# Kernel optimization log

Hardware: AMD Instinct MI355X
Metric: run time of the kernel (lower is better)

Reference implementation:

```python
import jax, jax.numpy as jnp
import numpy as np

E = 8        # num_experts
TOP_K = 2    # num_experts_per_tok
H = 2048     # hidden_size
I = 1408     # moe_intermediate_size

def setup_inputs() -> dict:
    key = jax.random.key(0)
    k0, k1, k2, k3, k4 = jax.random.split(key, 5)
    hidden_states = jax.random.normal(k0, (2, 2048, H), dtype=jnp.float32)
    gate_w = jax.random.normal(k1, (E, H), dtype=jnp.float32) * 0.02   # router: Linear(H, E)
    wg = jax.random.normal(k2, (E, I, H), dtype=jnp.float32) * 0.02    # gate_proj per expert
    wu = jax.random.normal(k3, (E, I, H), dtype=jnp.float32) * 0.02    # up_proj per expert
    wd = jax.random.normal(k4, (E, H, I), dtype=jnp.float32) * 0.02    # down_proj per expert
    return {"hidden_states": hidden_states, "gate_w": gate_w, "wg": wg, "wu": wu, "wd": wd}

def reference(hidden_states, gate_w, wg, wu, wd):
    b, s, h = hidden_states.shape
    x = hidden_states.reshape(-1, h)                      # [T, H]
    router_logits = x @ gate_w.T                          # [T, E]
    routing_weights = jax.nn.softmax(router_logits.astype(jnp.float32), axis=-1)
    topk_weight, topk_idx = jax.lax.top_k(routing_weights, TOP_K)   # [T, K]
    topk_weight = topk_weight / jnp.sum(topk_weight, axis=-1, keepdims=True)
    # per-token combine weight for each expert: w[t,e] = sum_k topk_weight[t,k] * [topk_idx[t,k]==e]
    comb = jnp.sum(jax.nn.one_hot(topk_idx, E, dtype=x.dtype) * topk_weight[..., None].astype(x.dtype), axis=1)  # [T, E]
    # compute each expert on all tokens (dense faithful equivalent of masked dispatch), combine with comb
    def expert_out(e):
        g = x @ wg[e].T                                   # [T, I]
        u = x @ wu[e].T                                   # [T, I]
        return (jax.nn.silu(g) * u) @ wd[e].T             # [T, H]
    y = jnp.zeros_like(x)
    for e in range(E):  # small fixed expert count
        y = y + expert_out(e) * comb[:, e:e+1]
    final = y.reshape(b, s, h)
    return final, router_logits.astype(hidden_states.dtype)
```

## Files before the change

kernel.cpp:

```cpp
#include <hip/hip_runtime.h>

#define NTOK 4096
#define NEXP 8
#define HD 2048
#define ID 1408

typedef unsigned short u16;
typedef __attribute__((ext_vector_type(8))) short short8;
typedef __attribute__((ext_vector_type(4))) short short4v;
typedef __attribute__((ext_vector_type(4))) float f32x4;
typedef const __attribute__((address_space(1))) void* gas_ptr;
typedef __attribute__((address_space(3))) void* las_ptr;

__device__ __forceinline__ u16 f2bf(float f) {
  unsigned int u = __float_as_uint(f);
  u += 0x7FFFu + ((u >> 16) & 1u);
  return (u16)(u >> 16);
}

__device__ __forceinline__ void async16(const u16* g, u16* l) {
  __builtin_amdgcn_global_load_lds((gas_ptr)g, (las_ptr)l, 16, 0, 0);
}

__global__ void cvt3_kernel(const float* __restrict__ s0, const float* __restrict__ s1,
                            const float* __restrict__ s2, u16* __restrict__ d0,
                            u16* __restrict__ d1, u16* __restrict__ d2, long n8each) {
  long i = (long)blockIdx.x * blockDim.x + threadIdx.x;
  const float* s; u16* d; long j;
  if (i < n8each)            { s = s0; d = d0; j = i; }
  else if (i < 2*n8each)     { s = s1; d = d1; j = i - n8each; }
  else if (i < 3*n8each)     { s = s2; d = d2; j = i - 2*n8each; }
  else return;
  const float4* s4 = (const float4*)s;
  float4 a = s4[2*j], b = s4[2*j+1];
  short8 o;
  o[0] = (short)f2bf(a.x); o[1] = (short)f2bf(a.y);
  o[2] = (short)f2bf(a.z); o[3] = (short)f2bf(a.w);
  o[4] = (short)f2bf(b.x); o[5] = (short)f2bf(b.y);
  o[6] = (short)f2bf(b.z); o[7] = (short)f2bf(b.w);
  *(short8*)(d + 8*j) = o;
}

__global__ void router_kernel(const float* __restrict__ x, const float* __restrict__ gw,
                              u16* __restrict__ xb,
                              float* __restrict__ logits, int* __restrict__ cnt,
                              int* __restrict__ ptok, float* __restrict__ pw) {
  int t = blockIdx.x * 4 + (threadIdx.x >> 6);
  int lane = threadIdx.x & 63;
  if (t >= NTOK) return;
  const float4* xr = (const float4*)(x + (size_t)t * HD);
  u16* xbr = xb + (size_t)t * HD;
  float dot[NEXP];
#pragma unroll
  for (int e = 0; e < NEXP; ++e) dot[e] = 0.f;
#pragma unroll
  for (int c = 0; c < 8; ++c) {
    float4 xv = xr[c*64 + lane];
    short4v o;
    o[0] = (short)f2bf(xv.x); o[1] = (short)f2bf(xv.y);
    o[2] = (short)f2bf(xv.z); o[3] = (short)f2bf(xv.w);
    *(short4v*)(xbr + (c*64 + lane)*4) = o;
#pragma unroll
    for (int e = 0; e < NEXP; ++e) {
      float4 gv = ((const float4*)(gw + e*HD))[c*64 + lane];
      dot[e] += xv.x*gv.x + xv.y*gv.y + xv.z*gv.z + xv.w*gv.w;
    }
  }
#pragma unroll
  for (int off = 32; off > 0; off >>= 1) {
#pragma unroll
    for (int e = 0; e < NEXP; ++e) dot[e] += __shfl_xor(dot[e], off);
  }
  if (lane < NEXP) logits[(size_t)t*NEXP + lane] = dot[lane];
  if (lane == 0) {
    float mx = dot[0];
#pragma unroll
    for (int e = 1; e < NEXP; ++e) mx = fmaxf(mx, dot[e]);
    float p[NEXP];
#pragma unroll
    for (int e = 0; e < NEXP; ++e) p[e] = __expf(dot[e] - mx);
    int e0 = 0;
#pragma unroll
    for (int e = 1; e < NEXP; ++e) if (p[e] > p[e0]) e0 = e;
    int e1 = (e0 == 0) ? 1 : 0;
#pragma unroll
    for (int e = 0; e < NEXP; ++e) if (e != e0 && p[e] > p[e1]) e1 = e;
    float denom = p[e0] + p[e1];
    int pos0 = atomicAdd(&cnt[e0], 1);
    ptok[e0*NTOK + pos0] = t; pw[e0*NTOK + pos0] = p[e0] / denom;
    int pos1 = atomicAdd(&cnt[e1], 1);
    ptok[e1*NTOK + pos1] = t; pw[e1*NTOK + pos1] = p[e1] / denom;
  }
}

__global__ void prefix_kernel(const int* __restrict__ cnt, int* __restrict__ offs) {
  if (threadIdx.x == 0) {
    int a = 0;
    for (int e = 0; e < NEXP; ++e) { offs[e] = a; a += cnt[e]; }
  }
}

__global__ __launch_bounds__(256, 2) void gemm1_kernel(
    const u16* __restrict__ xb, const u16* __restrict__ wgb, const u16* __restrict__ wub,
    const int* __restrict__ cnt, const int* __restrict__ offs,
    const int* __restrict__ ptok, u16* __restrict__ hbuf) {
  int e = blockIdx.z, mt = blockIdx.y, nt = blockIdx.x;
  int c = cnt[e];
  if (mt * 128 >= c) return;
  int off = offs[e];

  __shared__ u16 sA[128*64], sBg[128*64], sBu[128*64];

  int tid = threadIdx.x;
  int r  = tid >> 3;
  int cq = tid & 7;
  int cx = (cq ^ (r & 7)) * 8;

  const u16* ga[4];
#pragma unroll
  for (int p = 0; p < 4; ++p) {
    int s = mt*128 + r + p*32;
    int t = ptok[e*NTOK + (s < c ? s : 0)];
    ga[p] = xb + (size_t)t*HD + cx;
  }
  int n0 = nt*128 + r;
  const u16* gg = wgb + ((size_t)e*ID + n0)*HD + cx;
  const u16* gu = wub + ((size_t)e*ID + n0)*HD + cx;

  int lane = tid & 63, wv = tid >> 6, wr = wv >> 1, wc = wv & 1;
  int fm = lane & 15, kg = lane >> 4;
  int sw = fm & 7;

  f32x4 accg[4][4], accu[4][4];
#pragma unroll
  for (int i = 0; i < 4; ++i)
#pragma unroll
    for (int j = 0; j < 4; ++j) {
      accg[i][j] = {0.f, 0.f, 0.f, 0.f};
      accu[i][j] = {0.f, 0.f, 0.f, 0.f};
    }

  for (int k0 = 0; k0 < HD; k0 += 64) {
#pragma unroll
    for (int p = 0; p < 4; ++p) {
      async16(ga[p] + k0,                 sA  + p*2048 + tid*8);
      async16(gg + (size_t)p*32*HD + k0,  sBg + p*2048 + tid*8);
      async16(gu + (size_t)p*32*HD + k0,  sBu + p*2048 + tid*8);
    }
    __syncthreads();
#pragma unroll
    for (int h = 0; h < 2; ++h) {
      int co = ((kg + 4*h) ^ sw) * 8;
      short8 af[4], bg[4], bu[4];
#pragma unroll
      for (int i = 0; i < 4; ++i)
        af[i] = *(const short8*)(sA + (wr*64 + i*16 + fm)*64 + co);
#pragma unroll
      for (int j = 0; j < 4; ++j) {
        bg[j] = *(const short8*)(sBg + (wc*64 + j*16 + fm)*64 + co);
        bu[j] = *(const short8*)(sBu + (wc*64 + j*16 + fm)*64 + co);
      }
#pragma unroll
      for (int i = 0; i < 4; ++i)
#pragma unroll
        for (int j = 0; j < 4; ++j) {
          accg[i][j] = __builtin_amdgcn_mfma_f32_16x16x32_bf16(af[i], bg[j], accg[i][j], 0, 0, 0);
          accu[i][j] = __builtin_amdgcn_mfma_f32_16x16x32_bf16(af[i], bu[j], accu[i][j], 0, 0, 0);
        }
    }
    __syncthreads();
  }

#pragma unroll
  for (int i = 0; i < 4; ++i) {
#pragma unroll
    for (int rr = 0; rr < 4; ++rr) {
      int slot = mt*128 + wr*64 + i*16 + kg*4 + rr;
      if (slot < c) {
        size_t rowb = (size_t)(off + slot) * ID + nt*128 + wc*64 + fm;
#pragma unroll
        for (int j = 0; j < 4; ++j) {
          float gv = accg[i][j][rr], uv = accu[i][j][rr];
          float hh = gv * uv / (1.f + __expf(-gv));
          hbuf[rowb + (size_t)j*16] = f2bf(hh);
        }
      }
    }
  }
}

__global__ __launch_bounds__(256, 3) void gemm2_kernel(
    const u16* __restrict__ hbuf, const u16* __restrict__ wdb,
    const int* __restrict__ cnt, const int* __restrict__ offs,
    const int* __restrict__ ptok, const float* __restrict__ pw,
    float* __restrict__ out) {
  int e = blockIdx.z, mt = blockIdx.y, nt = blockIdx.x;
  int c = cnt[e];
  if (mt * 128 >= c) return;
  int off = offs[e];

  __shared__ u16 sA[128*64], sB[128*64];

  int tid = threadIdx.x;
  int r  = tid >> 3;
  int cq = tid & 7;
  int cx = (cq ^ (r & 7)) * 8;

  const u16* ga[4];
#pragma unroll
  for (int p = 0; p < 4; ++p) {
    int s = mt*128 + r + p*32;
    ga[p] = hbuf + (size_t)(off + (s < c ? s : 0))*ID + cx;
  }
  int n0 = nt*128 + r;
  const u16* gb = wdb + ((size_t)e*HD + n0)*ID + cx;

  int lane = tid & 63, wv = tid >> 6, wr = wv >> 1, wc = wv & 1;
  int fm = lane & 15, kg = lane >> 4;
  int sw = fm & 7;

  f32x4 acc[4][4];
#pragma unroll
  for (int i = 0; i < 4; ++i)
#pragma unroll
    for (int j = 0; j < 4; ++j) acc[i][j] = {0.f, 0.f, 0.f, 0.f};

  for (int k0 = 0; k0 < ID; k0 += 64) {
#pragma unroll
    for (int p = 0; p < 4; ++p) {
      async16(ga[p] + k0,                sA + p*2048 + tid*8);
      async16(gb + (size_t)p*32*ID + k0, sB + p*2048 + tid*8);
    }
    __syncthreads();
#pragma unroll
    for (int h = 0; h < 2; ++h) {
      int co = ((kg + 4*h) ^ sw) * 8;
      short8 af[4], bf[4];
#pragma unroll
      for (int i = 0; i < 4; ++i)
        af[i] = *(const short8*)(sA + (wr*64 + i*16 + fm)*64 + co);
#pragma unroll
      for (int j = 0; j < 4; ++j)
        bf[j] = *(const short8*)(sB + (wc*64 + j*16 + fm)*64 + co);
#pragma unroll
      for (int i = 0; i < 4; ++i)
#pragma unroll
        for (int j = 0; j < 4; ++j)
          acc[i][j] = __builtin_amdgcn_mfma_f32_16x16x32_bf16(af[i], bf[j], acc[i][j], 0, 0, 0);
    }
    __syncthreads();
  }

#pragma unroll
  for (int i = 0; i < 4; ++i) {
#pragma unroll
    for (int rr = 0; rr < 4; ++rr) {
      int slot = mt*128 + wr*64 + i*16 + kg*4 + rr;
      if (slot < c) {
        int tok = ptok[e*NTOK + slot];
        float wgt = pw[e*NTOK + slot];
        float* orow = out + (size_t)tok*HD + nt*128 + wc*64 + fm;
#pragma unroll
        for (int j = 0; j < 4; ++j)
          atomicAdd(orow + j*16, wgt * acc[i][j][rr]);
      }
    }
  }
}

extern "C" void kernel_launch(void* const* d_in, const int* in_sizes, int n_in,
                              void* d_out, int out_size, void* d_ws, size_t ws_size,
                              hipStream_t stream) {
  const float* x  = (const float*)d_in[0];
  const float* gw = (const float*)d_in[1];
  const float* wg = (const float*)d_in[2];
  const float* wu = (const float*)d_in[3];
  const float* wd = (const float*)d_in[4];
  float* out = (float*)d_out;

  char* p = (char*)d_ws;
  u16*   xb   = (u16*)(p);
  u16*   wgb  = (u16*)(p + 16777216UL);
  u16*   wub  = (u16*)(p + 62914560UL);
  u16*   wdb  = (u16*)(p + 109051904UL);
  u16*   hbuf = (u16*)(p + 155189248UL);
  int*   ptok = (int*)(p + 178257920UL);
  float* pww  = (float*)(p + 178388992UL);
  int*   cnt  = (int*)(p + 178520064UL);
  int*   offs = (int*)(p + 178520320UL);

  hipMemsetAsync(out, 0, (size_t)NTOK * HD * sizeof(float), stream);
  hipMemsetAsync(cnt, 0, NEXP * sizeof(int), stream);

  long n8each = (long)NEXP * ID * HD / 8;
  cvt3_kernel<<<33792, 256, 0, stream>>>(wg, wu, wd, wgb, wub, wdb, n8each);

  router_kernel<<<1024, 256, 0, stream>>>(x, gw, xb, out + (size_t)NTOK * HD, cnt, ptok, pww);
  prefix_kernel<<<1, 64, 0, stream>>>(cnt, offs);

  gemm1_kernel<<<dim3(11, 32, 8), 256, 0, stream>>>(xb, wgb, wub, cnt, offs, ptok, hbuf);
  gemm2_kernel<<<dim3(16, 32, 8), 256, 0, stream>>>(hbuf, wdb, cnt, offs, ptok, pww, out);
}
```

Before: 652.3 us.

## Double-buffer GEMM k-loops and split fused gate/up GEMM into two kernels

Introduces a shared double-buffered k-loop that prefetches the next two LDS tiles with async global-to-LDS loads, uses explicit waitcnt/barrier placement, and raises MFMA priority around the matrix-multiply blocks. The fused gate+up GEMM is split into a gate kernel, which writes bf16 gate values to hbuf, and an up kernel, which reads them back and applies SiLU*up. The split lowers register and LDS pressure per kernel but rereads x tiles, costs an extra hbuf round trip, and rounds the gate values to bf16 before the activation. The down-projection kernel also reuses the pipelined loop, with occupancy reduced from 3 to 2 blocks.

```diff
diff --git a/kernel.cpp b/kernel.cpp
--- a/kernel.cpp
+++ b/kernel.cpp
@@ -16,6 +16,9 @@
   unsigned int u = __float_as_uint(f);
   u += 0x7FFFu + ((u >> 16) & 1u);
   return (u16)(u >> 16);
+}
+__device__ __forceinline__ float bf2f(u16 v) {
+  return __uint_as_float((unsigned int)v << 16);
 }
 
 __device__ __forceinline__ void async16(const u16* g, u16* l) {
@@ -100,8 +103,74 @@
   }
 }
 
-__global__ __launch_bounds__(256, 2) void gemm1_kernel(
-    const u16* __restrict__ xb, const u16* __restrict__ wgb, const u16* __restrict__ wub,
+template<int NT>
+__device__ __forceinline__ void kloop(
+    const u16* const ga[4], const u16* const gb[4],
+    u16* sA, u16* sB, int tid, int fm, int kg, int wr, int wc,
+    f32x4 (&acc)[4][4])
+{
+  const int sw = fm & 7;
+  const int ar = wr*64 + fm;
+  const int br = wc*64 + fm;
+
+#define ISSUE(buf, k0) do { \
+    _Pragma("unroll") \
+    for (int p = 0; p < 4; ++p) { \
+      async16(ga[p] + (k0), sA + (buf)*8192 + p*2048 + tid*8); \
+      async16(gb[p] + (k0), sB + (buf)*8192 + p*2048 + tid*8); \
+    } } while (0)
+
+  ISSUE(0, 0);
+  ISSUE(1, 64);
+  asm volatile("s_waitcnt vmcnt(8)" ::: "memory");
+  asm volatile("s_barrier" ::: "memory");
+
+  for (int t = 0; t < NT; ++t) {
+    const u16* bA = sA + (t & 1) * 8192;
+    const u16* bB = sB + (t & 1) * 8192;
+    short8 a0[4], b0[4];
+    {
+      int co = (kg ^ sw) * 8;
+#pragma unroll
+      for (int i = 0; i < 4; ++i) a0[i] = *(const short8*)(bA + (ar + i*16)*64 + co);
+#pragma unroll
+      for (int j = 0; j < 4; ++j) b0[j] = *(const short8*)(bB + (br + j*16)*64 + co);
+    }
+    asm volatile("s_barrier" ::: "memory");
+    __builtin_amdgcn_s_setprio(1);
+#pragma unroll
+    for (int i = 0; i < 4; ++i)
+#pragma unroll
+      for (int j = 0; j < 4; ++j)
+        acc[i][j] = __builtin_amdgcn_mfma_f32_16x16x32_bf16(a0[i], b0[j], acc[i][j], 0, 0, 0);
+    __builtin_amdgcn_s_setprio(0);
+    asm volatile("s_barrier" ::: "memory");
+    short8 a1[4], b1[4];
+    {
+      int co = ((kg + 4) ^ sw) * 8;
+#pragma unroll
+      for (int i = 0; i < 4; ++i) a1[i] = *(const short8*)(bA + (ar + i*16)*64 + co);
+#pragma unroll
+      for (int j = 0; j < 4; ++j) b1[j] = *(const short8*)(bB + (br + j*16)*64 + co);
+    }
+    asm volatile("s_barrier" ::: "memory");
+    if (t + 2 < NT) ISSUE((t & 1), (t + 2) * 64);
+    __builtin_amdgcn_s_setprio(1);
+#pragma unroll
+    for (int i = 0; i < 4; ++i)
+#pragma unroll
+      for (int j = 0; j < 4; ++j)
+        acc[i][j] = __builtin_amdgcn_mfma_f32_16x16x32_bf16(a1[i], b1[j], acc[i][j], 0, 0, 0);
+    __builtin_amdgcn_s_setprio(0);
+    if (t < NT - 2)       asm volatile("s_waitcnt vmcnt(8)" ::: "memory");
+    else if (t == NT - 2) asm volatile("s_waitcnt vmcnt(0)" ::: "memory");
+    asm volatile("s_barrier" ::: "memory");
+  }
+#undef ISSUE
+}
+
+__global__ __launch_bounds__(256, 2) void gemmg_kernel(
+    const u16* __restrict__ xb, const u16* __restrict__ wgb,
     const int* __restrict__ cnt, const int* __restrict__ offs,
     const int* __restrict__ ptok, u16* __restrict__ hbuf) {
   int e = blockIdx.z, mt = blockIdx.y, nt = blockIdx.x;
@@ -109,7 +178,7 @@
   if (mt * 128 >= c) return;
   int off = offs[e];
 
-  __shared__ u16 sA[128*64], sBg[128*64], sBu[128*64];
+  __shared__ u16 sA[2*128*64], sB[2*128*64];
 
   int tid = threadIdx.x;
   int r  = tid >> 3;
@@ -123,53 +192,21 @@
     int t = ptok[e*NTOK + (s < c ? s : 0)];
     ga[p] = xb + (size_t)t*HD + cx;
   }
-  int n0 = nt*128 + r;
-  const u16* gg = wgb + ((size_t)e*ID + n0)*HD + cx;
-  const u16* gu = wub + ((size_t)e*ID + n0)*HD + cx;
+  const u16* gb[4];
+#pragma unroll
+  for (int p = 0; p < 4; ++p)
+    gb[p] = wgb + ((size_t)e*ID + nt*128 + r + p*32)*HD + cx;
 
   int lane = tid & 63, wv = tid >> 6, wr = wv >> 1, wc = wv & 1;
   int fm = lane & 15, kg = lane >> 4;
-  int sw = fm & 7;
-
-  f32x4 accg[4][4], accu[4][4];
+
+  f32x4 acc[4][4];
 #pragma unroll
   for (int i = 0; i < 4; ++i)
 #pragma unroll
-    for (int j = 0; j < 4; ++j) {
-      accg[i][j] = {0.f, 0.f, 0.f, 0.f};
-      accu[i][j] = {0.f, 0.f, 0.f, 0.f};
-    }
-
-  for (int k0 = 0; k0 < HD; k0 += 64) {
-#pragma unroll
-    for (int p = 0; p < 4; ++p) {
-      async16(ga[p] + k0,                 sA  + p*2048 + tid*8);
-      async16(gg + (size_t)p*32*HD + k0,  sBg + p*2048 + tid*8);
-      async16(gu + (size_t)p*32*HD + k0,  sBu + p*2048 + tid*8);
-    }
-    __syncthreads();
-#pragma unroll
-    for (int h = 0; h < 2; ++h) {
-      int co = ((kg + 4*h) ^ sw) * 8;
-      short8 af[4], bg[4], bu[4];
-#pragma unroll
-      for (int i = 0; i < 4; ++i)
-        af[i] = *(const short8*)(sA + (wr*64 + i*16 + fm)*64 + co);
-#pragma unroll
-      for (int j = 0; j < 4; ++j) {
-        bg[j] = *(const short8*)(sBg + (wc*64 + j*16 + fm)*64 + co);
-        bu[j] = *(const short8*)(sBu + (wc*64 + j*16 + fm)*64 + co);
-      }
-#pragma unroll
-      for (int i = 0; i < 4; ++i)
-#pragma unroll
-        for (int j = 0; j < 4; ++j) {
-          accg[i][j] = __builtin_amdgcn_mfma_f32_16x16x32_bf16(af[i], bg[j], accg[i][j], 0, 0, 0);
-          accu[i][j] = __builtin_amdgcn_mfma_f32_16x16x32_bf16(af[i], bu[j], accu[i][j], 0, 0, 0);
-        }
-    }
-    __syncthreads();
-  }
+    for (int j = 0; j < 4; ++j) acc[i][j] = {0.f, 0.f, 0.f, 0.f};
+
+  kloop<HD/64>(ga, gb, sA, sB, tid, fm, kg, wr, wc, acc);
 
 #pragma unroll
   for (int i = 0; i < 4; ++i) {
@@ -179,9 +216,64 @@
       if (slot < c) {
         size_t rowb = (size_t)(off + slot) * ID + nt*128 + wc*64 + fm;
 #pragma unroll
+        for (int j = 0; j < 4; ++j)
+          hbuf[rowb + (size_t)j*16] = f2bf(acc[i][j][rr]);
+      }
+    }
+  }
+}
+
+__global__ __launch_bounds__(256, 2) void gemmu_kernel(
+    const u16* __restrict__ xb, const u16* __restrict__ wub,
+    const int* __restrict__ cnt, const int* __restrict__ offs,
+    const int* __restrict__ ptok, u16* __restrict__ hbuf) {
+  int e = blockIdx.z, mt = blockIdx.y, nt = blockIdx.x;
+  int c = cnt[e];
+  if (mt * 128 >= c) return;
+  int off = offs[e];
+
+  __shared__ u16 sA[2*128*64], sB[2*128*64];
+
+  int tid = threadIdx.x;
+  int r  = tid >> 3;
+  int cq = tid & 7;
+  int cx = (cq ^ (r & 7)) * 8;
+
+  const u16* ga[4];
+#pragma unroll
+  for (int p = 0; p < 4; ++p) {
+    int s = mt*128 + r + p*32;
+    int t = ptok[e*NTOK + (s < c ? s : 0)];
+    ga[p] = xb + (size_t)t*HD + cx;
+  }
+  const u16* gb[4];
+#pragma unroll
+  for (int p = 0; p < 4; ++p)
+    gb[p] = wub + ((size_t)e*ID + nt*128 + r + p*32)*HD + cx;
+
+  int lane = tid & 63, wv = tid >> 6, wr = wv >> 1, wc = wv & 1;
+  int fm = lane & 15, kg = lane >> 4;
+
+  f32x4 acc[4][4];
+#pragma unroll
+  for (int i = 0; i < 4; ++i)
+#pragma unroll
+    for (int j = 0; j < 4; ++j) acc[i][j] = {0.f, 0.f, 0.f, 0.f};
+
+  kloop<HD/64>(ga, gb, sA, sB, tid, fm, kg, wr, wc, acc);
+
+#pragma unroll
+  for (int i = 0; i < 4; ++i) {
+#pragma unroll
+    for (int rr = 0; rr < 4; ++rr) {
+      int slot = mt*128 + wr*64 + i*16 + kg*4 + rr;
+      if (slot < c) {
+        size_t rowb = (size_t)(off + slot) * ID + nt*128 + wc*64 + fm;
+#pragma unroll
         for (int j = 0; j < 4; ++j) {
-          float gv = accg[i][j][rr], uv = accu[i][j][rr];
-          float hh = gv * uv / (1.f + __expf(-gv));
+          float g32 = bf2f(hbuf[rowb + (size_t)j*16]);
+          float uv  = acc[i][j][rr];
+          float hh  = g32 * uv / (1.f + __expf(-g32));
           hbuf[rowb + (size_t)j*16] = f2bf(hh);
         }
       }
@@ -189,7 +281,7 @@
   }
 }
 
-__global__ __launch_bounds__(256, 3) void gemm2_kernel(
+__global__ __launch_bounds__(256, 2) void gemmd_kernel(
     const u16* __restrict__ hbuf, const u16* __restrict__ wdb,
     const int* __restrict__ cnt, const int* __restrict__ offs,
     const int* __restrict__ ptok, const float* __restrict__ pw,
@@ -199,7 +291,7 @@
   if (mt * 128 >= c) return;
   int off = offs[e];
 
-  __shared__ u16 sA[128*64], sB[128*64];
+  __shared__ u16 sA[2*128*64], sB[2*128*64];
 
   int tid = threadIdx.x;
   int r  = tid >> 3;
@@ -212,12 +304,13 @@
     int s = mt*128 + r + p*32;
     ga[p] = hbuf + (size_t)(off + (s < c ? s : 0))*ID + cx;
   }
-  int n0 = nt*128 + r;
-  const u16* gb = wdb + ((size_t)e*HD + n0)*ID + cx;
+  const u16* gb[4];
+#pragma unroll
+  for (int p = 0; p < 4; ++p)
+    gb[p] = wdb + ((size_t)e*HD + nt*128 + r + p*32)*ID + cx;
 
   int lane = tid & 63, wv = tid >> 6, wr = wv >> 1, wc = wv & 1;
   int fm = lane & 15, kg = lane >> 4;
-  int sw = fm & 7;
 
   f32x4 acc[4][4];
 #pragma unroll
@@ -225,31 +318,7 @@
 #pragma unroll
     for (int j = 0; j < 4; ++j) acc[i][j] = {0.f, 0.f, 0.f, 0.f};
 
-  for (int k0 = 0; k0 < ID; k0 += 64) {
-#pragma unroll
-    for (int p = 0; p < 4; ++p) {
-      async16(ga[p] + k0,                sA + p*2048 + tid*8);
-      async16(gb + (size_t)p*32*ID + k0, sB + p*2048 + tid*8);
-    }
-    __syncthreads();
-#pragma unroll
-    for (int h = 0; h < 2; ++h) {
-      int co = ((kg + 4*h) ^ sw) * 8;
-      short8 af[4], bf[4];
-#pragma unroll
-      for (int i = 0; i < 4; ++i)
-        af[i] = *(const short8*)(sA + (wr*64 + i*16 + fm)*64 + co);
-#pragma unroll
-      for (int j = 0; j < 4; ++j)
-        bf[j] = *(const short8*)(sB + (wc*64 + j*16 + fm)*64 + co);
-#pragma unroll
-      for (int i = 0; i < 4; ++i)
-#pragma unroll
-        for (int j = 0; j < 4; ++j)
-          acc[i][j] = __builtin_amdgcn_mfma_f32_16x16x32_bf16(af[i], bf[j], acc[i][j], 0, 0, 0);
-    }
-    __syncthreads();
-  }
+  kloop<ID/64>(ga, gb, sA, sB, tid, fm, kg, wr, wc, acc);
 
 #pragma unroll
   for (int i = 0; i < 4; ++i) {
@@ -298,6 +367,7 @@
   router_kernel<<<1024, 256, 0, stream>>>(x, gw, xb, out + (size_t)NTOK * HD, cnt, ptok, pww);
   prefix_kernel<<<1, 64, 0, stream>>>(cnt, offs);
 
-  gemm1_kernel<<<dim3(11, 32, 8), 256, 0, stream>>>(xb, wgb, wub, cnt, offs, ptok, hbuf);
-  gemm2_kernel<<<dim3(16, 32, 8), 256, 0, stream>>>(hbuf, wdb, cnt, offs, ptok, pww, out);
-}
+  gemmg_kernel<<<dim3(11, 32, 8), 256, 0, stream>>>(xb, wgb, cnt, offs, ptok, hbuf);
+  gemmu_kernel<<<dim3(11, 32, 8), 256, 0, stream>>>(xb, wub, cnt, offs, ptok, hbuf);
+  gemmd_kernel<<<dim3(16, 32, 8), 256, 0, stream>>>(hbuf, wdb, cnt, offs, ptok, pww, out);
+}
```

Measured after the change: 720.4 us. 10.4% more time.

## Enlarge MoE GEMM tiles to 256 rows with multi-stage LDS pipelining

Applied to the files above, without the earlier changes.

Both expert GEMMs now use 512-thread blocks with 256-row M tiles, which halves the grid along M. A shared templated K-loop issues the next stage's async global-to-LDS loads before computing on the current stage. gemm1 double-buffers, and gemm2 triple-buffers using explicit vmcnt waits and raw barriers, and MFMA sections run at raised wave priority. The aim is to hide global load latency behind MFMA work and improve data reuse per block, at the cost of more LDS per block, lower occupancy, and more padded rows for experts with few tokens.

```diff
diff --git a/kernel.cpp b/kernel.cpp
--- a/kernel.cpp
+++ b/kernel.cpp
@@ -100,36 +100,118 @@
   }
 }
 
-__global__ __launch_bounds__(256, 2) void gemm1_kernel(
+template<int NT, int NSTG, int DUAL>
+__device__ __forceinline__ void kloop256(
+    const u16* const ga[4], const u16* const gb0[2], const u16* const gb1[2],
+    u16* sA, u16* sB0, u16* sB1,
+    int tid, int wr, int wc, int fm, int kg,
+    f32x4 (&acc0)[4][4], f32x4 (&acc1)[4][4])
+{
+  const int swz = fm & 7;
+
+#define STG(st, k0) do { \
+    _Pragma("unroll") \
+    for (int q = 0; q < 4; ++q) \
+      async16(ga[q] + (k0), sA + (st)*16384 + q*4096 + tid*8); \
+    _Pragma("unroll") \
+    for (int q = 0; q < 2; ++q) \
+      async16(gb0[q] + (k0), sB0 + (st)*8192 + q*4096 + tid*8); \
+    if (DUAL) { \
+      _Pragma("unroll") \
+      for (int q = 0; q < 2; ++q) \
+        async16(gb1[q] + (k0), sB1 + (st)*8192 + q*4096 + tid*8); \
+    } } while (0)
+
+  STG(0, 0);
+  if (NSTG == 3) {
+    STG(1, 64);
+    asm volatile("s_waitcnt vmcnt(6)" ::: "memory");
+    __builtin_amdgcn_s_barrier();
+    __builtin_amdgcn_sched_barrier(0);
+  } else {
+    __syncthreads();
+  }
+
+  for (int t = 0; t < NT; ++t) {
+    int pre = t + NSTG - 1;
+    if (pre < NT) STG(pre % NSTG, pre * 64);
+    const u16* bA  = sA  + (t % NSTG) * 16384;
+    const u16* bB0 = sB0 + (t % NSTG) * 8192;
+    const u16* bB1 = sB1 + (t % NSTG) * 8192;
+#pragma unroll
+    for (int ks = 0; ks < 2; ++ks) {
+      int co = ((ks*4 + kg) ^ swz) * 8;
+      short8 av[4], b0[4], b1[4];
+#pragma unroll
+      for (int j = 0; j < 4; ++j) {
+        b0[j] = *(const short8*)(bB0 + (wc*64 + j*16 + fm)*64 + co);
+        if (DUAL) b1[j] = *(const short8*)(bB1 + (wc*64 + j*16 + fm)*64 + co);
+      }
+#pragma unroll
+      for (int i = 0; i < 4; ++i)
+        av[i] = *(const short8*)(bA + (wr*64 + i*16 + fm)*64 + co);
+      __builtin_amdgcn_s_setprio(1);
+#pragma unroll
+      for (int i = 0; i < 4; ++i)
+#pragma unroll
+        for (int j = 0; j < 4; ++j) {
+          acc0[i][j] = __builtin_amdgcn_mfma_f32_16x16x32_bf16(av[i], b0[j], acc0[i][j], 0, 0, 0);
+          if (DUAL)
+            acc1[i][j] = __builtin_amdgcn_mfma_f32_16x16x32_bf16(av[i], b1[j], acc1[i][j], 0, 0, 0);
+        }
+      __builtin_amdgcn_s_setprio(0);
+    }
+    if (t + 1 < NT) {
+      if (NSTG == 3 && t + 2 < NT) {
+        asm volatile("s_waitcnt vmcnt(6)" ::: "memory");
+        __builtin_amdgcn_s_barrier();
+        __builtin_amdgcn_sched_barrier(0);
+      } else if (NSTG == 3) {
+        asm volatile("s_waitcnt vmcnt(0)" ::: "memory");
+        __builtin_amdgcn_s_barrier();
+        __builtin_amdgcn_sched_barrier(0);
+      } else {
+        __syncthreads();
+      }
+    }
+  }
+#undef STG
+}
+
+__global__ __launch_bounds__(512, 2) void gemm1_kernel(
     const u16* __restrict__ xb, const u16* __restrict__ wgb, const u16* __restrict__ wub,
     const int* __restrict__ cnt, const int* __restrict__ offs,
     const int* __restrict__ ptok, u16* __restrict__ hbuf) {
   int e = blockIdx.z, mt = blockIdx.y, nt = blockIdx.x;
   int c = cnt[e];
-  if (mt * 128 >= c) return;
+  if (mt * 256 >= c) return;
   int off = offs[e];
 
-  __shared__ u16 sA[128*64], sBg[128*64], sBu[128*64];
+  __shared__ u16 sA[2*256*64], sBg[2*128*64], sBu[2*128*64];
 
   int tid = threadIdx.x;
-  int r  = tid >> 3;
+  int r5 = tid >> 3;
   int cq = tid & 7;
-  int cx = (cq ^ (r & 7)) * 8;
+  int cx = (cq ^ (r5 & 7)) * 8;
 
   const u16* ga[4];
 #pragma unroll
-  for (int p = 0; p < 4; ++p) {
-    int s = mt*128 + r + p*32;
+  for (int q = 0; q < 4; ++q) {
+    int s = mt*256 + q*64 + r5;
     int t = ptok[e*NTOK + (s < c ? s : 0)];
-    ga[p] = xb + (size_t)t*HD + cx;
-  }
-  int n0 = nt*128 + r;
-  const u16* gg = wgb + ((size_t)e*ID + n0)*HD + cx;
-  const u16* gu = wub + ((size_t)e*ID + n0)*HD + cx;
+    ga[q] = xb + (size_t)t*HD + cx;
+  }
+  const u16* gbg[2];
+  const u16* gbu[2];
+#pragma unroll
+  for (int q = 0; q < 2; ++q) {
+    int n = nt*128 + q*64 + r5;
+    gbg[q] = wgb + ((size_t)e*ID + n)*HD + cx;
+    gbu[q] = wub + ((size_t)e*ID + n)*HD + cx;
+  }
 
   int lane = tid & 63, wv = tid >> 6, wr = wv >> 1, wc = wv & 1;
   int fm = lane & 15, kg = lane >> 4;
-  int sw = fm & 7;
 
   f32x4 accg[4][4], accu[4][4];
 #pragma unroll
@@ -140,42 +222,13 @@
       accu[i][j] = {0.f, 0.f, 0.f, 0.f};
     }
 
-  for (int k0 = 0; k0 < HD; k0 += 64) {
-#pragma unroll
-    for (int p = 0; p < 4; ++p) {
-      async16(ga[p] + k0,                 sA  + p*2048 + tid*8);
-      async16(gg + (size_t)p*32*HD + k0,  sBg + p*2048 + tid*8);
-      async16(gu + (size_t)p*32*HD + k0,  sBu + p*2048 + tid*8);
-    }
-    __syncthreads();
-#pragma unroll
-    for (int h = 0; h < 2; ++h) {
-      int co = ((kg + 4*h) ^ sw) * 8;
-      short8 af[4], bg[4], bu[4];
-#pragma unroll
-      for (int i = 0; i < 4; ++i)
-        af[i] = *(const short8*)(sA + (wr*64 + i*16 + fm)*64 + co);
-#pragma unroll
-      for (int j = 0; j < 4; ++j) {
-        bg[j] = *(const short8*)(sBg + (wc*64 + j*16 + fm)*64 + co);
-        bu[j] = *(const short8*)(sBu + (wc*64 + j*16 + fm)*64 + co);
-      }
-#pragma unroll
-      for (int i = 0; i < 4; ++i)
-#pragma unroll
-        for (int j = 0; j < 4; ++j) {
-          accg[i][j] = __builtin_amdgcn_mfma_f32_16x16x32_bf16(af[i], bg[j], accg[i][j], 0, 0, 0);
-          accu[i][j] = __builtin_amdgcn_mfma_f32_16x16x32_bf16(af[i], bu[j], accu[i][j], 0, 0, 0);
-        }
-    }
-    __syncthreads();
-  }
+  kloop256<HD/64, 2, 1>(ga, gbg, gbu, sA, sBg, sBu, tid, wr, wc, fm, kg, accg, accu);
 
 #pragma unroll
   for (int i = 0; i < 4; ++i) {
 #pragma unroll
     for (int rr = 0; rr < 4; ++rr) {
-      int slot = mt*128 + wr*64 + i*16 + kg*4 + rr;
+      int slot = mt*256 + wr*64 + i*16 + kg*4 + rr;
       if (slot < c) {
         size_t rowb = (size_t)(off + slot) * ID + nt*128 + wc*64 + fm;
 #pragma unroll
@@ -189,73 +242,52 @@
   }
 }
 
-__global__ __launch_bounds__(256, 3) void gemm2_kernel(
+__global__ __launch_bounds__(512, 2) void gemm2_kernel(
     const u16* __restrict__ hbuf, const u16* __restrict__ wdb,
     const int* __restrict__ cnt, const int* __restrict__ offs,
     const int* __restrict__ ptok, const float* __restrict__ pw,
     float* __restrict__ out) {
   int e = blockIdx.z, mt = blockIdx.y, nt = blockIdx.x;
   int c = cnt[e];
-  if (mt * 128 >= c) return;
+  if (mt * 256 >= c) return;
   int off = offs[e];
 
-  __shared__ u16 sA[128*64], sB[128*64];
+  __shared__ u16 sA[3*256*64], sB[3*128*64];
 
   int tid = threadIdx.x;
-  int r  = tid >> 3;
+  int r5 = tid >> 3;
   int cq = tid & 7;
-  int cx = (cq ^ (r & 7)) * 8;
+  int cx = (cq ^ (r5 & 7)) * 8;
 
   const u16* ga[4];
 #pragma unroll
-  for (int p = 0; p < 4; ++p) {
-    int s = mt*128 + r + p*32;
-    ga[p] = hbuf + (size_t)(off + (s < c ? s : 0))*ID + cx;
-  }
-  int n0 = nt*128 + r;
-  const u16* gb = wdb + ((size_t)e*HD + n0)*ID + cx;
+  for (int q = 0; q < 4; ++q) {
+    int s = mt*256 + q*64 + r5;
+    ga[q] = hbuf + (size_t)(off + (s < c ? s : 0))*ID + cx;
+  }
+  const u16* gb[2];
+#pragma unroll
+  for (int q = 0; q < 2; ++q) {
+    int n = nt*128 + q*64 + r5;
+    gb[q] = wdb + ((size_t)e*HD + n)*ID + cx;
+  }
 
   int lane = tid & 63, wv = tid >> 6, wr = wv >> 1, wc = wv & 1;
   int fm = lane & 15, kg = lane >> 4;
-  int sw = fm & 7;
-
-  f32x4 acc[4][4];
+
+  f32x4 acc[4][4], dummy[4][4];
 #pragma unroll
   for (int i = 0; i < 4; ++i)
 #pragma unroll
     for (int j = 0; j < 4; ++j) acc[i][j] = {0.f, 0.f, 0.f, 0.f};
 
-  for (int k0 = 0; k0 < ID; k0 += 64) {
-#pragma unroll
-    for (int p = 0; p < 4; ++p) {
-      async16(ga[p] + k0,                sA + p*2048 + tid*8);
-      async16(gb + (size_t)p*32*ID + k0, sB + p*2048 + tid*8);
-    }
-    __syncthreads();
-#pragma unroll
-    for (int h = 0; h < 2; ++h) {
-      int co = ((kg + 4*h) ^ sw) * 8;
-      short8 af[4], bf[4];
-#pragma unroll
-      for (int i = 0; i < 4; ++i)
-        af[i] = *(const short8*)(sA + (wr*64 + i*16 + fm)*64 + co);
-#pragma unroll
-      for (int j = 0; j < 4; ++j)
-        bf[j] = *(const short8*)(sB + (wc*64 + j*16 + fm)*64 + co);
-#pragma unroll
-      for (int i = 0; i < 4; ++i)
-#pragma unroll
-        for (int j = 0; j < 4; ++j)
-          acc[i][j] = __builtin_amdgcn_mfma_f32_16x16x32_bf16(af[i], bf[j], acc[i][j], 0, 0, 0);
-    }
-    __syncthreads();
-  }
+  kloop256<ID/64, 3, 0>(ga, gb, gb, sA, sB, sB, tid, wr, wc, fm, kg, acc, dummy);
 
 #pragma unroll
   for (int i = 0; i < 4; ++i) {
 #pragma unroll
     for (int rr = 0; rr < 4; ++rr) {
-      int slot = mt*128 + wr*64 + i*16 + kg*4 + rr;
+      int slot = mt*256 + wr*64 + i*16 + kg*4 + rr;
       if (slot < c) {
         int tok = ptok[e*NTOK + slot];
         float wgt = pw[e*NTOK + slot];
@@ -298,6 +330,6 @@
   router_kernel<<<1024, 256, 0, stream>>>(x, gw, xb, out + (size_t)NTOK * HD, cnt, ptok, pww);
   prefix_kernel<<<1, 64, 0, stream>>>(cnt, offs);
 
-  gemm1_kernel<<<dim3(11, 32, 8), 256, 0, stream>>>(xb, wgb, wub, cnt, offs, ptok, hbuf);
-  gemm2_kernel<<<dim3(16, 32, 8), 256, 0, stream>>>(hbuf, wdb, cnt, offs, ptok, pww, out);
-}
+  gemm1_kernel<<<dim3(11, 16, 8), 512, 0, stream>>>(xb, wgb, wub, cnt, offs, ptok, hbuf);
+  gemm2_kernel<<<dim3(16, 16, 8), 512, 0, stream>>>(hbuf, wdb, cnt, offs, ptok, pww, out);
+}
```

Result: slower. 689.0 us (+5.6%).
